# Performance work log

Measured on AMD Instinct MI355X. Metric: run time of the kernel, lower is better.

Reference implementation:

```python
import jax, jax.numpy as jnp
import numpy as np

SPATIAL_SHAPES = np.array([[100, 100], [50, 50], [25, 25], [13, 13]], dtype=np.int32)
EMBED, NH, NL, NP = 256, 8, 4, 4
HD = EMBED // NH  # 32


def setup_inputs() -> dict:
    key = jax.random.key(0)
    ks = jax.random.split(key, 12)
    bs, nq = 4, 4000
    nv = int((SPATIAL_SHAPES[:, 0] * SPATIAL_SHAPES[:, 1]).sum())  # 13294
    s_lin = 1.0 / np.sqrt(EMBED)  # xavier-ish scale
    s_small = 0.02                # offsets/weights heads start near init
    return {
        "query": jax.random.normal(ks[0], (bs, nq, EMBED), jnp.float32),
        "value": jax.random.normal(ks[1], (bs, nv, EMBED), jnp.float32),
        "reference_points": jax.random.uniform(ks[2], (bs, nq, NL, 2), jnp.float32),
        "spatial_shapes": jnp.asarray(SPATIAL_SHAPES),
        "W_off": jax.random.normal(ks[3], (EMBED, NH * NL * NP * 2), jnp.float32) * s_small,
        "b_off": jax.random.normal(ks[4], (NH * NL * NP * 2,), jnp.float32) * s_small,
        "W_attn": jax.random.normal(ks[5], (EMBED, NH * NL * NP), jnp.float32) * s_small,
        "b_attn": jax.random.normal(ks[6], (NH * NL * NP,), jnp.float32) * s_small,
        "W_val": jax.random.normal(ks[7], (EMBED, EMBED), jnp.float32) * s_lin,
        "b_val": jnp.zeros((EMBED,), jnp.float32),
        "W_out": jax.random.normal(ks[8], (EMBED, EMBED), jnp.float32) * s_lin,
        "b_out": jnp.zeros((EMBED,), jnp.float32),
    }


def _bilinear_sample(val_l, H, W, x, y):
    """grid_sample(mode=bilinear, padding=zeros, align_corners=False) equivalent.
    val_l: [bs, nh, H*W, hd]; x, y: [bs, nh, nq, np] pixel-space coords.
    Returns [bs, nh, nq, np, hd]."""
    x0 = jnp.floor(x)
    y0 = jnp.floor(y)
    bs, nh, nq, npts = x.shape
    out = 0.0
    for dx, dy in ((0, 0), (1, 0), (0, 1), (1, 1)):
        xi = x0 + dx
        yi = y0 + dy
        w = (1.0 - jnp.abs(x - xi)) * (1.0 - jnp.abs(y - yi))
        valid = (xi >= 0) & (xi < W) & (yi >= 0) & (yi < H)
        idx = (jnp.clip(yi, 0, H - 1) * W + jnp.clip(xi, 0, W - 1)).astype(jnp.int32)
        g = jnp.take_along_axis(val_l, idx.reshape(bs, nh, nq * npts, 1), axis=2)
        g = g.reshape(bs, nh, nq, npts, -1)
        out = out + g * (w * valid.astype(w.dtype))[..., None]
    return out


def reference(query, value, reference_points, spatial_shapes,
              W_off, b_off, W_attn, b_attn, W_val, b_val, W_out, b_out):
    shapes = np.asarray(spatial_shapes)  # static level shapes
    bs, nq, _ = query.shape
    # value projection -> per-head layout [bs, nh, nv, hd]
    v = (value @ W_val + b_val).reshape(bs, -1, NH, HD).transpose(0, 2, 1, 3)
    # sampling offsets and attention weights from query
    off = (query @ W_off + b_off).reshape(bs, nq, NH, NL, NP, 2)
    attn = jax.nn.softmax((query @ W_attn + b_attn).reshape(bs, nq, NH, NL * NP), axis=-1)
    attn = attn.reshape(bs, nq, NH, NL, NP)
    # normalized sampling locations; normalizer = (W, H) per level
    normalizer = jnp.asarray(np.stack([shapes[:, 1], shapes[:, 0]], -1), jnp.float32)
    loc = reference_points[:, :, None, :, None, :] + off / normalizer[None, None, None, :, None, :]
    out = jnp.zeros((bs, NH, nq, HD), query.dtype)
    start = 0
    for l in range(NL):
        H, W = int(shapes[l, 0]), int(shapes[l, 1])
        val_l = v[:, :, start:start + H * W, :]
        # pixel coords with align_corners=False: p = loc*size - 0.5
        x = loc[:, :, :, l, :, 0].transpose(0, 2, 1, 3) * W - 0.5  # [bs,nh,nq,np]
        y = loc[:, :, :, l, :, 1].transpose(0, 2, 1, 3) * H - 0.5
        sampled = _bilinear_sample(val_l, H, W, x, y)  # [bs,nh,nq,np,hd]
        out = out + jnp.einsum('bhqpd,bqhp->bhqd', sampled, attn[:, :, :, l, :])
        start += H * W
    out = out.transpose(0, 2, 1, 3).reshape(bs, nq, EMBED)
    return out @ W_out + b_out
```

## Files before the change

kernel.cpp:

```cpp
#include <hip/hip_runtime.h>
#include <hip/hip_bf16.h>

#define EMBED 256
#define NH 8
#define NL 4
#define NP 4
#define HD 32
#define BS 4
#define NQ 4000
#define NV 13294

using f32x4   = __attribute__((ext_vector_type(4))) float;
using bf16x8  = __attribute__((ext_vector_type(8))) short;

__device__ __forceinline__ float bf2f_lo(unsigned u) {
    union { unsigned u; float f; } x; x.u = u << 16; return x.f;
}
__device__ __forceinline__ float bf2f_hi(unsigned u) {
    union { unsigned u; float f; } x; x.u = u & 0xffff0000u; return x.f;
}
__device__ __forceinline__ unsigned short f2bf(float f) {
    union { float f; unsigned u; } x; x.f = f;
    unsigned u = x.u;
    return (unsigned short)((u + 0x7fffu + ((u >> 16) & 1u)) >> 16);
}
__device__ __forceinline__ unsigned cvtpk(float lo, float hi) {
    unsigned r;
    asm("v_cvt_pk_bf16_f32 %0, %1, %2" : "=v"(r) : "v"(lo), "v"(hi));
    return r;
}

__device__ __forceinline__ void async16(const void* g, void* l) {
    __builtin_amdgcn_global_load_lds(
        (const __attribute__((address_space(1))) void*)g,
        (__attribute__((address_space(3))) void*)l, 16, 0, 0);
}

template<int N> __device__ __forceinline__ void wait_vmcnt() {
    if constexpr (N == 0)      asm volatile("s_waitcnt vmcnt(0)" ::: "memory");
    else if constexpr (N == 2) asm volatile("s_waitcnt vmcnt(2)" ::: "memory");
    else if constexpr (N == 3) asm volatile("s_waitcnt vmcnt(3)" ::: "memory");
}

__global__ __launch_bounds__(256) void msda_prep_k(
    const float* __restrict__ W_val, const float* __restrict__ W_out,
    const float* __restrict__ W_off, const float* __restrict__ W_attn,
    const float* __restrict__ b_off, const float* __restrict__ b_attn,
    unsigned short* __restrict__ Wt_val, unsigned short* __restrict__ Wt_out,
    unsigned short* __restrict__ Wt_qa, float* __restrict__ b_qa)
{
    int i = blockIdx.x * 256 + threadIdx.x;
    if (i < 384) b_qa[i] = (i < 256) ? b_off[i] : b_attn[i - 256];
    if (i < 65536) {
        int r = i >> 8, c = i & 255;
        Wt_val[c * 256 + r] = f2bf(W_val[i]);
    } else if (i < 131072) {
        int j = i - 65536, r = j >> 8, c = j & 255;
        Wt_out[c * 256 + r] = f2bf(W_out[j]);
    } else if (i < 229376) {
        int j = i - 131072;
        int n = j >> 8, k = j & 255;
        float v = (n < 256) ? W_off[k * 256 + n] : W_attn[k * 128 + (n - 256)];
        Wt_qa[j] = f2bf(v);
    }
}

template<int EPI, bool ABF16>
__device__ __forceinline__ void gemm_body(
    char* lds,
    const void* __restrict__ Ap,
    const unsigned short* __restrict__ Bt,
    const float* __restrict__ bias,
    void* __restrict__ out,
    int M, int N, int mblk, int nblk)
{
    constexpr int K = 256, C = 8;
    constexpr int NI = 2;
    constexpr int ABYTES = 128 * 32 * 2;
    constexpr int BUFB   = ABYTES + 128 * 32 * 2;
    constexpr int LOPS   = ABF16 ? 1 : 2;

    const int m0 = mblk * 128, n0 = nblk * 128;
    const int tid  = threadIdx.x;
    const int w    = tid >> 6;
    const int lane = tid & 63;
    const int quad = lane >> 4;
    const int l16  = lane & 15;
    const int wm   = (w & 1) * 64;
    const int wn   = (w >> 1) * 32;

    const int ar  = tid >> 2;
    const int arg = min(m0 + ar, M - 1);
    const int ak  = (tid & 3) * 8;
    const float*          afp = (const float*)Ap          + (size_t)arg * K + ak;
    const unsigned short* abp = (const unsigned short*)Ap + (size_t)arg * K + ak;

    const char* bgp = (const char*)(Bt + (size_t)(n0 + w * 16 + (lane >> 2)) * K)
                      + (lane & 3) * 16;

    auto issueB = [&](int c, int kb) {
        async16(bgp + c * 64, lds + kb * BUFB + ABYTES + w * 1024);
    };

    float4 aLoR[2], aHiR[2];
    bf16x8 aRegR[2];
    auto loadA = [&](int c) {
        const int p = c & 1;
        if constexpr (ABF16) {
            aRegR[p] = *(const bf16x8*)(abp + c * 32);
        } else {
            aLoR[p] = *(const float4*)(afp + c * 32);
            aHiR[p] = *(const float4*)(afp + c * 32 + 4);
        }
    };
    auto writeA = [&](int c) {
        const int p = c & 1;
        unsigned short* dst = (unsigned short*)(lds + (c % 3) * BUFB) + ar * 32 + ak;
        if constexpr (ABF16) {
            *(bf16x8*)dst = aRegR[p];
        } else {
            union { unsigned u[4]; bf16x8 v; } t;
            t.u[0] = cvtpk(aLoR[p].x, aLoR[p].y); t.u[1] = cvtpk(aLoR[p].z, aLoR[p].w);
            t.u[2] = cvtpk(aHiR[p].x, aHiR[p].y); t.u[3] = cvtpk(aHiR[p].z, aHiR[p].w);
            *(bf16x8*)dst = t.v;
        }
    };

    f32x4 acc[4][NI];
#pragma unroll
    for (int a = 0; a < 4; a++)
#pragma unroll
        for (int b = 0; b < NI; b++) acc[a][b] = (f32x4){0.f, 0.f, 0.f, 0.f};

    loadA(0); issueB(0, 0); loadA(1); issueB(1, 1);
    writeA(0);

#pragma unroll
    for (int c = 0; c < C; c++) {
        if (c < C - 1) wait_vmcnt<LOPS + 1>(); else wait_vmcnt<0>();
        asm volatile("s_waitcnt lgkmcnt(0)" ::: "memory");
        __builtin_amdgcn_s_barrier();
        __builtin_amdgcn_sched_barrier(0);
        if (c + 2 < C) { loadA(c + 2); issueB(c + 2, (c + 2) % 3); }

        const char* aL = lds + (c % 3) * BUFB;
        const char* bL = aL + ABYTES;
        bf16x8 af[4], bfr[NI];
#pragma unroll
        for (int mi = 0; mi < 4; mi++)
            af[mi] = *(const bf16x8*)(aL + (wm + mi * 16 + l16) * 64 + quad * 16);
#pragma unroll
        for (int ni = 0; ni < NI; ni++)
            bfr[ni] = *(const bf16x8*)(bL + (wn + ni * 16 + l16) * 64 + quad * 16);

        if (c + 1 < C) writeA(c + 1);

#pragma unroll
        for (int mi = 0; mi < 4; mi++)
#pragma unroll
            for (int ni = 0; ni < NI; ni++)
                acc[mi][ni] = __builtin_amdgcn_mfma_f32_16x16x32_bf16(af[mi], bfr[ni], acc[mi][ni], 0, 0, 0);
    }

    if constexpr (EPI == 0) {
        __syncthreads();
        unsigned short* cs = (unsigned short*)lds;
#pragma unroll
        for (int ni = 0; ni < NI; ni++) {
            int cl = wn + ni * 16 + l16;
            float bvv = bias[n0 + cl];
#pragma unroll
            for (int mi = 0; mi < 4; mi++)
#pragma unroll
                for (int r = 0; r < 4; r++) {
                    int ml = wm + mi * 16 + quad * 4 + r;
                    cs[ml * 136 + cl] = f2bf(acc[mi][ni][r] + bvv);
                }
        }
        __syncthreads();
        const int seg = tid >> 7, rr = tid & 127;
        const int m = m0 + rr;
        if (m < M) {
            const int b   = m / NV;
            const int pix = m - b * NV;
            const int h   = (n0 >> 5) + seg;
            char* dst = (char*)out + (((size_t)b * 8 + h) * NV + pix) * 64;
            const uint4* s = (const uint4*)&cs[rr * 136 + seg * 32];
#pragma unroll
            for (int j = 0; j < 4; j++) ((uint4*)dst)[j] = s[j];
        }
    } else {
#pragma unroll
        for (int ni = 0; ni < NI; ni++) {
            int cc = n0 + wn + ni * 16 + l16;
            float bvv = bias[cc];
#pragma unroll
            for (int mi = 0; mi < 4; mi++)
#pragma unroll
                for (int r = 0; r < 4; r++) {
                    int m = m0 + wm + mi * 16 + quad * 4 + r;
                    if (m >= M) continue;
                    ((float*)out)[(size_t)m * N + cc] = acc[mi][ni][r] + bvv;
                }
        }
    }
}

__global__ __launch_bounds__(512) void msda_gemm_vq_k(
    const float* __restrict__ value, const float* __restrict__ query,
    const unsigned short* __restrict__ Wt_val, const unsigned short* __restrict__ Wt_qa,
    const float* __restrict__ b_val, const float* __restrict__ b_qa,
    unsigned short* __restrict__ v_buf, float* __restrict__ oa_buf)
{
    extern __shared__ char lds[];
    const int bx = blockIdx.x;
    if (bx < 832) {
        gemm_body<0, false>(lds, value, Wt_val, b_val, v_buf,
                            BS * NV, 256, bx >> 1, bx & 1);
    } else {
        const int j = bx - 832;
        const int mb = j / 3;
        gemm_body<1, false>(lds, query, Wt_qa, b_qa, oa_buf,
                            BS * NQ, 384, mb, j - mb * 3);
    }
}

__global__ __launch_bounds__(512) void msda_gemm_out_k(
    const unsigned short* __restrict__ t_buf,
    const unsigned short* __restrict__ Wt_out,
    const float* __restrict__ b_out,
    float* __restrict__ out)
{
    extern __shared__ char lds[];
    const int bx = blockIdx.x;
    gemm_body<1, true>(lds, t_buf, Wt_out, b_out, out,
                       BS * NQ, 256, bx >> 1, bx & 1);
}

__global__ __launch_bounds__(256) void msda_sampler_k(
    const float* __restrict__ refpts,
    const float* __restrict__ oa_buf,
    const unsigned short* __restrict__ v_buf,
    unsigned short* __restrict__ t_out)
{
    __shared__ float  oa_s[4][384];
    __shared__ float  ref_s[4][8];
    __shared__ float4 wtab[528];
    __shared__ int4   itab[528];

    const int tid = threadIdx.x;
    const int q0  = blockIdx.x * 4;

    {
        const float4* src = (const float4*)(oa_buf + (size_t)q0 * 384);
        float4* dst = (float4*)&oa_s[0][0];
        dst[tid] = src[tid];
        if (tid < 128) dst[256 + tid] = src[256 + tid];
        if (tid < 32) ((float*)ref_s)[tid] = refpts[q0 * 8 + tid];
    }
    __syncthreads();

    const int HWs[4]    = {100, 50, 25, 13};
    const int starts[4] = {0, 10000, 12500, 13125};
#pragma unroll
    for (int it = 0; it < 2; it++) {
        int s  = tid + it * 256;
        int i  = s & 15;
        int h  = (s >> 4) & 7;
        int ql = s >> 7;
        int l  = i >> 2, p = i & 3;
        float logit = oa_s[ql][256 + h * 16 + i];
        float m = logit;
#pragma unroll
        for (int off = 1; off < 16; off <<= 1) m = fmaxf(m, __shfl_xor(m, off, 64));
        float e = __expf(logit - m);
        float sum = e;
#pragma unroll
        for (int off = 1; off < 16; off <<= 1) sum += __shfl_xor(sum, off, 64);
        float a = e / sum;

        int Wl = HWs[l];
        float fW = (float)Wl;
        float rx = ref_s[ql][l * 2], ry = ref_s[ql][l * 2 + 1];
        float offx = oa_s[ql][h * 32 + l * 8 + p * 2];
        float offy = oa_s[ql][h * 32 + l * 8 + p * 2 + 1];
        float x = rx * fW + offx - 0.5f;
        float y = ry * fW + offy - 0.5f;
        float xf = floorf(x), yf = floorf(y);
        float fx = x - xf, fy = y - yf;
        int x0 = (int)xf, y0 = (int)yf;
        int x1 = x0 + 1, y1 = y0 + 1;
        float wx0 = (x0 >= 0 && x0 < Wl) ? (1.f - fx) : 0.f;
        float wx1 = (x1 >= 0 && x1 < Wl) ? fx : 0.f;
        float wy0 = (y0 >= 0 && y0 < Wl) ? (1.f - fy) : 0.f;
        float wy1 = (y1 >= 0 && y1 < Wl) ? fy : 0.f;
        int x0c = min(max(x0, 0), Wl - 1), x1c = min(max(x1, 0), Wl - 1);
        int y0c = min(max(y0, 0), Wl - 1), y1c = min(max(y1, 0), Wl - 1);
        int r0 = starts[l] + y0c * Wl, r1 = starts[l] + y1c * Wl;
        int ti = i * 33 + ql * 8 + h;
        wtab[ti] = make_float4(wx0 * wy0 * a, wx1 * wy0 * a, wx0 * wy1 * a, wx1 * wy1 * a);
        itab[ti] = make_int4(r0 + x0c, r0 + x1c, r1 + x0c, r1 + x1c);
    }
    __syncthreads();

    const int dg = tid & 7, h = (tid >> 3) & 7, ql = tid >> 6;
    const int q = q0 + ql;
    const int b = q / NQ;
    const char* base = (const char*)v_buf + ((size_t)(b * 8 + h)) * NV * 64 + dg * 8;
    const int tbase = ql * 8 + h;

    float a0 = 0.f, a1 = 0.f, a2 = 0.f, a3 = 0.f;
#pragma unroll
    for (int lp = 0; lp < 16; lp++) {
        float4 wv = wtab[lp * 33 + tbase];
        int4   ix = itab[lp * 33 + tbase];
        uint2 s0 = *(const uint2*)(base + ((unsigned)ix.x << 6));
        uint2 s1 = *(const uint2*)(base + ((unsigned)ix.y << 6));
        uint2 s2 = *(const uint2*)(base + ((unsigned)ix.z << 6));
        uint2 s3 = *(const uint2*)(base + ((unsigned)ix.w << 6));
        a0 += wv.x * bf2f_lo(s0.x); a1 += wv.x * bf2f_hi(s0.x);
        a2 += wv.x * bf2f_lo(s0.y); a3 += wv.x * bf2f_hi(s0.y);
        a0 += wv.y * bf2f_lo(s1.x); a1 += wv.y * bf2f_hi(s1.x);
        a2 += wv.y * bf2f_lo(s1.y); a3 += wv.y * bf2f_hi(s1.y);
        a0 += wv.z * bf2f_lo(s2.x); a1 += wv.z * bf2f_hi(s2.x);
        a2 += wv.z * bf2f_lo(s2.y); a3 += wv.z * bf2f_hi(s2.y);
        a0 += wv.w * bf2f_lo(s3.x); a1 += wv.w * bf2f_hi(s3.x);
        a2 += wv.w * bf2f_lo(s3.y); a3 += wv.w * bf2f_hi(s3.y);
    }
    unsigned o0 = (unsigned)f2bf(a0) | ((unsigned)f2bf(a1) << 16);
    unsigned o1 = (unsigned)f2bf(a2) | ((unsigned)f2bf(a3) << 16);
    uint2 o = {o0, o1};
    *(uint2*)(t_out + (size_t)q * 256 + h * 32 + dg * 4) = o;
}

extern "C" void kernel_launch(void* const* d_in, const int* in_sizes, int n_in,
                              void* d_out, int out_size, void* d_ws, size_t ws_size,
                              hipStream_t stream) {
    const float* query  = (const float*)d_in[0];
    const float* value  = (const float*)d_in[1];
    const float* refpts = (const float*)d_in[2];
    const float* W_off  = (const float*)d_in[4];
    const float* b_off  = (const float*)d_in[5];
    const float* W_attn = (const float*)d_in[6];
    const float* b_attn = (const float*)d_in[7];
    const float* W_val  = (const float*)d_in[8];
    const float* b_val  = (const float*)d_in[9];
    const float* W_out  = (const float*)d_in[10];
    const float* b_out  = (const float*)d_in[11];

    char* wsp = (char*)d_ws;
    size_t o = 0;
    auto carve = [&](size_t bytes) -> void* {
        void* p = wsp + o; o += (bytes + 255) & ~(size_t)255; return p;
    };
    unsigned short* Wt_val = (unsigned short*)carve(256 * 256 * 2);
    unsigned short* Wt_out = (unsigned short*)carve(256 * 256 * 2);
    unsigned short* Wt_qa  = (unsigned short*)carve(384 * 256 * 2);
    float*          b_qa   = (float*)carve(384 * 4);
    unsigned short* v_buf  = (unsigned short*)carve((size_t)BS * NH * NV * 32 * 2);
    float*          oa_buf = (float*)carve((size_t)BS * NQ * 384 * 4);
    unsigned short* t_buf  = (unsigned short*)carve((size_t)BS * NQ * EMBED * 2);

    msda_prep_k<<<896, 256, 0, stream>>>(W_val, W_out, W_off, W_attn,
                                         b_off, b_attn, Wt_val, Wt_out, Wt_qa, b_qa);

    msda_gemm_vq_k<<<832 + 375, 512, 49152, stream>>>(value, query, Wt_val, Wt_qa,
                                                      b_val, b_qa, v_buf, oa_buf);
    msda_sampler_k<<<(BS * NQ) / 4, 256, 0, stream>>>(refpts, oa_buf, v_buf, t_buf);
    msda_gemm_out_k<<<250, 512, 49152, stream>>>(t_buf, Wt_out, b_out, (float*)d_out);
}
```

Baseline: 196.0 us.

## Split bilinear gather by x-corner with 16-byte loads and shuffle reduction

The sampler now stores per-sample row weights, combined x weights and two row base indices instead of four corner weights and four indices. Lanes are split into two groups, one per x-corner column (x0 or x0+1); each lane loads 16 bytes (8 bf16 channels) from each of two rows. Partial sums from the two groups are combined with a cross-lane shuffle, and only one group writes the output. The aim is fewer, wider gather instructions and less LDS table traffic, at the cost of a shuffle reduction, half the lanes being idle at the store, and clamp logic that folds the two x weights into an adjacent pixel pair.

```diff
diff --git a/kernel.cpp b/kernel.cpp
--- a/kernel.cpp
+++ b/kernel.cpp
@@ -246,7 +246,7 @@
     __shared__ float  oa_s[4][384];
     __shared__ float  ref_s[4][8];
     __shared__ float4 wtab[528];
-    __shared__ int4   itab[528];
+    __shared__ int2   itab[528];
 
     const int tid = threadIdx.x;
     const int q0  = blockIdx.x * 4;
@@ -297,40 +297,54 @@
         int x0c = min(max(x0, 0), Wl - 1), x1c = min(max(x1, 0), Wl - 1);
         int y0c = min(max(y0, 0), Wl - 1), y1c = min(max(y1, 0), Wl - 1);
         int r0 = starts[l] + y0c * Wl, r1 = starts[l] + y1c * Wl;
+
+        int xb = min(max(x0, 0), Wl - 2);
+        float wlo = ((x0c == xb)     ? wx0 : 0.f) + ((x1c == xb)     ? wx1 : 0.f);
+        float whi = ((x0c == xb + 1) ? wx0 : 0.f) + ((x1c == xb + 1) ? wx1 : 0.f);
+
         int ti = i * 33 + ql * 8 + h;
-        wtab[ti] = make_float4(wx0 * wy0 * a, wx1 * wy0 * a, wx0 * wy1 * a, wx1 * wy1 * a);
-        itab[ti] = make_int4(r0 + x0c, r0 + x1c, r1 + x0c, r1 + x1c);
+        wtab[ti] = make_float4(wy0 * a, wy1 * a, wlo, whi);
+        itab[ti] = make_int2(r0 + xb, r1 + xb);
     }
     __syncthreads();
 
-    const int dg = tid & 7, h = (tid >> 3) & 7, ql = tid >> 6;
+    const int dg4 = tid & 3, xc = (tid >> 2) & 1, h = (tid >> 3) & 7, ql = tid >> 6;
     const int q = q0 + ql;
     const int b = q / NQ;
-    const char* base = (const char*)v_buf + ((size_t)(b * 8 + h)) * NV * 64 + dg * 8;
+    const char* base = (const char*)v_buf + ((size_t)(b * 8 + h)) * NV * 64 + dg4 * 16;
     const int tbase = ql * 8 + h;
 
     float a0 = 0.f, a1 = 0.f, a2 = 0.f, a3 = 0.f;
+    float a4 = 0.f, a5 = 0.f, a6 = 0.f, a7 = 0.f;
 #pragma unroll
     for (int lp = 0; lp < 16; lp++) {
         float4 wv = wtab[lp * 33 + tbase];
-        int4   ix = itab[lp * 33 + tbase];
-        uint2 s0 = *(const uint2*)(base + ((unsigned)ix.x << 6));
-        uint2 s1 = *(const uint2*)(base + ((unsigned)ix.y << 6));
-        uint2 s2 = *(const uint2*)(base + ((unsigned)ix.z << 6));
-        uint2 s3 = *(const uint2*)(base + ((unsigned)ix.w << 6));
-        a0 += wv.x * bf2f_lo(s0.x); a1 += wv.x * bf2f_hi(s0.x);
-        a2 += wv.x * bf2f_lo(s0.y); a3 += wv.x * bf2f_hi(s0.y);
-        a0 += wv.y * bf2f_lo(s1.x); a1 += wv.y * bf2f_hi(s1.x);
-        a2 += wv.y * bf2f_lo(s1.y); a3 += wv.y * bf2f_hi(s1.y);
-        a0 += wv.z * bf2f_lo(s2.x); a1 += wv.z * bf2f_hi(s2.x);
-        a2 += wv.z * bf2f_lo(s2.y); a3 += wv.z * bf2f_hi(s2.y);
-        a0 += wv.w * bf2f_lo(s3.x); a1 += wv.w * bf2f_hi(s3.x);
-        a2 += wv.w * bf2f_lo(s3.y); a3 += wv.w * bf2f_hi(s3.y);
-    }
-    unsigned o0 = (unsigned)f2bf(a0) | ((unsigned)f2bf(a1) << 16);
-    unsigned o1 = (unsigned)f2bf(a2) | ((unsigned)f2bf(a3) << 16);
-    uint2 o = {o0, o1};
-    *(uint2*)(t_out + (size_t)q * 256 + h * 32 + dg * 4) = o;
+        int2   iv = itab[lp * 33 + tbase];
+        uint4 s0 = *(const uint4*)(base + ((unsigned)(iv.x + xc) << 6));
+        uint4 s1 = *(const uint4*)(base + ((unsigned)(iv.y + xc) << 6));
+        float wx = xc ? wv.w : wv.z;
+        float w0 = wx * wv.x, w1 = wx * wv.y;
+        a0 += w0 * bf2f_lo(s0.x); a1 += w0 * bf2f_hi(s0.x);
+        a2 += w0 * bf2f_lo(s0.y); a3 += w0 * bf2f_hi(s0.y);
+        a4 += w0 * bf2f_lo(s0.z); a5 += w0 * bf2f_hi(s0.z);
+        a6 += w0 * bf2f_lo(s0.w); a7 += w0 * bf2f_hi(s0.w);
+        a0 += w1 * bf2f_lo(s1.x); a1 += w1 * bf2f_hi(s1.x);
+        a2 += w1 * bf2f_lo(s1.y); a3 += w1 * bf2f_hi(s1.y);
+        a4 += w1 * bf2f_lo(s1.z); a5 += w1 * bf2f_hi(s1.z);
+        a6 += w1 * bf2f_lo(s1.w); a7 += w1 * bf2f_hi(s1.w);
+    }
+    a0 += __shfl_xor(a0, 4, 64); a1 += __shfl_xor(a1, 4, 64);
+    a2 += __shfl_xor(a2, 4, 64); a3 += __shfl_xor(a3, 4, 64);
+    a4 += __shfl_xor(a4, 4, 64); a5 += __shfl_xor(a5, 4, 64);
+    a6 += __shfl_xor(a6, 4, 64); a7 += __shfl_xor(a7, 4, 64);
+    if (xc == 0) {
+        uint4 o;
+        o.x = (unsigned)f2bf(a0) | ((unsigned)f2bf(a1) << 16);
+        o.y = (unsigned)f2bf(a2) | ((unsigned)f2bf(a3) << 16);
+        o.z = (unsigned)f2bf(a4) | ((unsigned)f2bf(a5) << 16);
+        o.w = (unsigned)f2bf(a6) | ((unsigned)f2bf(a7) << 16);
+        *(uint4*)(t_out + (size_t)q * 256 + h * 32 + dg4 * 8) = o;
+    }
 }
 
 extern "C" void kernel_launch(void* const* d_in, const int* in_sizes, int n_in,
```

New measurement: 193.6 us. Within noise of the previous version (-1.2%).
